# Performance work log

Hardware: AMD Instinct MI355X
Metric: run time of the kernel (lower is better)

The kernel has to match this reference:

```python
import jax, jax.numpy as jnp
import numpy as np

B, L, IN_DIM, H, DK, DV = 4, 512, 256, 8, 32, 32
TEMP = DK ** 0.5  # temperature = d_k ** 0.5
LN_EPS = 1e-6


def setup_inputs() -> dict:
    key = jax.random.key(0)
    ks = jax.random.split(key, 5)
    s = 0.05
    return {
        "x": jax.random.normal(ks[0], (B, L, IN_DIM), jnp.float32),
        "w_q": jax.random.normal(ks[1], (IN_DIM, H * DK), jnp.float32) * s,
        "w_k": jax.random.normal(ks[2], (IN_DIM, H * DK), jnp.float32) * s,
        "w_v": jax.random.normal(ks[3], (IN_DIM, H * DV), jnp.float32) * s,
        "w_fc": jax.random.normal(ks[4], (H * DV, IN_DIM), jnp.float32) * s,
        "ln_gamma": jnp.ones((IN_DIM,), jnp.float32),
        "ln_beta": jnp.zeros((IN_DIM,), jnp.float32),
    }


def reference(x, w_q, w_k, w_v, w_fc, ln_gamma, ln_beta):
    # LayerNorm (biased variance, eps inside sqrt, as in torch.nn.LayerNorm)
    mu = jnp.mean(x, axis=-1, keepdims=True)
    var = jnp.var(x, axis=-1, keepdims=True)
    xn = (x - mu) / jnp.sqrt(var + LN_EPS) * ln_gamma + ln_beta
    residual = xn

    # Projections; torch layout after transpose(1,3) is [B, d, H, L]; per-head slice is [B, d, L].
    # We use [B, H, d, L] which yields identical per-head tensors (vectorized over heads).
    q = (xn @ w_q).reshape(B, L, H, DK).transpose(0, 2, 3, 1) / TEMP  # [B,H,DK,L]
    k = (xn @ w_k).reshape(B, L, H, DK).transpose(0, 2, 3, 1)          # [B,H,DK,L]
    v = (xn @ w_v).reshape(B, L, H, DV).transpose(0, 2, 3, 1)          # [B,H,DV,L]

    # L1 distance scores (note the source's index convention):
    # attn[b,h,i,j] = mean_d |q[b,h,d,j] - k[b,h,d,i]|   -> [B,H,L,L]
    attn = jnp.mean(jnp.abs(q[:, :, :, None, :] - k[:, :, :, :, None]), axis=2)
    attn = jax.nn.softmax(attn, axis=-1)

    # out[b,h,d,i] = sum_j v[b,h,d,j] * attn[b,h,i,j]   (torch: bmm(v, attn^T))
    out = jnp.einsum('bhdj,bhij->bhdi', v, attn)  # [B,H,DV,L]
    out = out.reshape(B, H * DV, L).transpose(0, 2, 1)  # head-major concat -> [B,L,H*DV]
    out = out @ w_fc + residual  # use_gamma=False path; dropout is identity at eval

    # extract_attn_map (no_grad in source)
    am = jax.lax.stop_gradient(attn)
    am = jnp.mean(am, axis=1)          # mean over heads -> [B,L,L]
    am = jnp.sum(am, axis=1)           # sum over key axis -> [B,L]
    mn = jnp.min(am, axis=1, keepdims=True)
    mx = jnp.max(am, axis=1, keepdims=True)
    am = (am - mn) / (mx - mn)
    return out, am
```

## Files before the change

kernel.cpp:

```cpp
#include <hip/hip_runtime.h>
#include <hip/hip_fp16.h>
#include <math.h>

#define BATCH 4
#define SEQ   512
#define IND   256
#define NH    8
#define DKV   32
#define BH    32
#define NTOK  2048

typedef __attribute__((ext_vector_type(8))) short short8v;
typedef __attribute__((ext_vector_type(4))) float floatx4;

__device__ __forceinline__ unsigned f2bf1(float f) {
    unsigned u = __builtin_bit_cast(unsigned, f);
    return (u + 0x7fffu + ((u >> 16) & 1u)) >> 16;
}
__device__ __forceinline__ unsigned f2bf2(float lo, float hi) {
    return f2bf1(lo) | (f2bf1(hi) << 16);
}
__device__ __forceinline__ __half2 habs2_(__half2 x) {
    unsigned u = __builtin_bit_cast(unsigned, x) & 0x7fff7fffu;
    return __builtin_bit_cast(__half2, u);
}
__device__ __forceinline__ __half2 shfl_xor_h2(__half2 x, int m) {
    float f = __builtin_bit_cast(float, x);
    f = __shfl_xor(f, m, 64);
    return __builtin_bit_cast(__half2, f);
}

__global__ __launch_bounds__(256) void lnproj_kernel(
        const float* __restrict__ x,
        const float* __restrict__ gamma, const float* __restrict__ beta,
        const float* __restrict__ wq, const float* __restrict__ wk,
        const float* __restrict__ wv,
        float* __restrict__ xn, float* __restrict__ am,
        __half* __restrict__ Q, __half* __restrict__ K, __half* __restrict__ V) {
    __shared__ __align__(16) unsigned short As[64][264];
    __shared__ __align__(16) unsigned short Bs[2][64][40];
    const int t = threadIdx.x;
    const int m0 = blockIdx.x * 64;
    const int y = blockIdx.y;
    const int which = y >> 2;
    const int n0 = (y & 3) * 64;
    const float* W = (which == 0) ? wq : (which == 1) ? wk : wv;
    __half* O = (which == 0) ? Q : (which == 1) ? K : V;

    {
        const int r = t >> 2, q = t & 3;
        const float* xr = x + (m0 + r) * IND + q * 64;
        float4 xv[16];
        float s = 0.0f, s2 = 0.0f;
        #pragma unroll
        for (int i = 0; i < 16; i++) {
            xv[i] = *(const float4*)&xr[i * 4];
            s  += xv[i].x + xv[i].y + xv[i].z + xv[i].w;
            s2 += xv[i].x * xv[i].x + xv[i].y * xv[i].y
                + xv[i].z * xv[i].z + xv[i].w * xv[i].w;
        }
        s  += __shfl_xor(s, 1, 64);  s  += __shfl_xor(s, 2, 64);
        s2 += __shfl_xor(s2, 1, 64); s2 += __shfl_xor(s2, 2, 64);
        float mu = s * (1.0f / IND);
        float var = s2 * (1.0f / IND) - mu * mu;
        float rinv = rsqrtf(var + 1e-6f);
        const bool dox = (y == 0);
        if (dox && t < 64) am[m0 + t] = 0.0f;
        #pragma unroll
        for (int i = 0; i < 8; i++) {
            float4 a = xv[2 * i], bv = xv[2 * i + 1];
            float4 g0 = *(const float4*)&gamma[q * 64 + i * 8];
            float4 g1 = *(const float4*)&gamma[q * 64 + i * 8 + 4];
            float4 b0 = *(const float4*)&beta[q * 64 + i * 8];
            float4 b1 = *(const float4*)&beta[q * 64 + i * 8 + 4];
            float4 n0v, n1v;
            n0v.x = (a.x - mu) * rinv * g0.x + b0.x;
            n0v.y = (a.y - mu) * rinv * g0.y + b0.y;
            n0v.z = (a.z - mu) * rinv * g0.z + b0.z;
            n0v.w = (a.w - mu) * rinv * g0.w + b0.w;
            n1v.x = (bv.x - mu) * rinv * g1.x + b1.x;
            n1v.y = (bv.y - mu) * rinv * g1.y + b1.y;
            n1v.z = (bv.z - mu) * rinv * g1.z + b1.z;
            n1v.w = (bv.w - mu) * rinv * g1.w + b1.w;
            if (dox) {
                *(float4*)&xn[(m0 + r) * IND + q * 64 + i * 8] = n0v;
                *(float4*)&xn[(m0 + r) * IND + q * 64 + i * 8 + 4] = n1v;
            }
            uint4 pk;
            pk.x = f2bf2(n0v.x, n0v.y); pk.y = f2bf2(n0v.z, n0v.w);
            pk.z = f2bf2(n1v.x, n1v.y); pk.w = f2bf2(n1v.z, n1v.w);
            *(uint4*)&As[r][q * 64 + i * 8] = pk;
        }
    }

    const int w = t >> 6, l = t & 63;
    const int wm = (w >> 1) * 32, wn = (w & 1) * 32;
    const int fr = l & 15, fg = l >> 4;
    floatx4 acc[2][2];
    #pragma unroll
    for (int i = 0; i < 2; i++)
        #pragma unroll
        for (int j = 0; j < 2; j++) acc[i][j] = (floatx4)(0.0f);

    const int kl = t >> 4, nq = t & 15;
    auto stageB = [&](int kt, int buf) {
        float4 b0 = *(const float4*)&W[(kt * 32 + kl) * IND + n0 + nq * 4];
        float4 b1 = *(const float4*)&W[(kt * 32 + 16 + kl) * IND + n0 + nq * 4];
        Bs[buf][nq * 4 + 0][kl] = (unsigned short)f2bf1(b0.x);
        Bs[buf][nq * 4 + 1][kl] = (unsigned short)f2bf1(b0.y);
        Bs[buf][nq * 4 + 2][kl] = (unsigned short)f2bf1(b0.z);
        Bs[buf][nq * 4 + 3][kl] = (unsigned short)f2bf1(b0.w);
        Bs[buf][nq * 4 + 0][kl + 16] = (unsigned short)f2bf1(b1.x);
        Bs[buf][nq * 4 + 1][kl + 16] = (unsigned short)f2bf1(b1.y);
        Bs[buf][nq * 4 + 2][kl + 16] = (unsigned short)f2bf1(b1.z);
        Bs[buf][nq * 4 + 3][kl + 16] = (unsigned short)f2bf1(b1.w);
    };
    stageB(0, 0);
    __syncthreads();
    #pragma unroll
    for (int kt = 0; kt < 8; kt++) {
        if (kt < 7) stageB(kt + 1, (kt + 1) & 1);
        const int buf = kt & 1;
        short8v a0 = *(const short8v*)&As[wm + fr][kt * 32 + fg * 8];
        short8v a1 = *(const short8v*)&As[wm + 16 + fr][kt * 32 + fg * 8];
        short8v b0 = *(const short8v*)&Bs[buf][wn + fr][fg * 8];
        short8v b1 = *(const short8v*)&Bs[buf][wn + 16 + fr][fg * 8];
        acc[0][0] = __builtin_amdgcn_mfma_f32_16x16x32_bf16(a0, b0, acc[0][0], 0, 0, 0);
        acc[0][1] = __builtin_amdgcn_mfma_f32_16x16x32_bf16(a0, b1, acc[0][1], 0, 0, 0);
        acc[1][0] = __builtin_amdgcn_mfma_f32_16x16x32_bf16(a1, b0, acc[1][0], 0, 0, 0);
        acc[1][1] = __builtin_amdgcn_mfma_f32_16x16x32_bf16(a1, b1, acc[1][1], 0, 0, 0);
        __syncthreads();
    }

    const float scale = (which == 0) ? 0.17677669529663687f : 1.0f;
    #pragma unroll
    for (int mi = 0; mi < 2; mi++)
        #pragma unroll
        for (int ni = 0; ni < 2; ni++)
            #pragma unroll
            for (int reg = 0; reg < 4; reg++) {
                int row = m0 + wm + mi * 16 + fg * 4 + reg;
                int col = n0 + wn + ni * 16 + fr;
                int b = row >> 9, ll = row & 511;
                int h = col >> 5, d = col & 31;
                O[(((b << 3) + h) * SEQ + ll) * DKV + d] =
                    __float2half_rn(acc[mi][ni][reg] * scale);
            }
}

__global__ __launch_bounds__(256) void attn_kernel(
        const __half* __restrict__ Qh, const __half* __restrict__ Kh,
        const __half* __restrict__ Vh, float* __restrict__ attn_out,
        float* __restrict__ am) {
    __shared__ __align__(16) __half Th[2][128][40];
    const int t = threadIdx.x;
    const int gy = blockIdx.y;
    const int i0 = blockIdx.x * 16;
    const int b = gy >> 3, h = gy & 7;
    const __half* Qb = Qh + gy * SEQ * DKV;
    const __half* Kb = Kh + gy * SEQ * DKV;
    const __half* Vb = Vh + gy * SEQ * DKV;
    const int g = t >> 5, jl = t & 31;
    const int r0 = t >> 2, ch = t & 3;

    __half2 ka[16], kb[16];
    {
        const float4* pa = (const float4*)(Kb + (i0 + g) * DKV);
        const float4* pb = (const float4*)(Kb + (i0 + g + 8) * DKV);
        #pragma unroll
        for (int c = 0; c < 4; c++) {
            float4 va = pa[c], vb = pb[c];
            const __half2* ha = (const __half2*)&va;
            const __half2* hb = (const __half2*)&vb;
            #pragma unroll
            for (int k = 0; k < 4; k++) { ka[c*4+k] = ha[k]; kb[c*4+k] = hb[k]; }
        }
    }

    float vals_a[16], vals_b[16];
    float4 pre0, pre1;

    pre0 = *(const float4*)(Qb + r0 * DKV + ch * 8);
    pre1 = *(const float4*)(Qb + (r0 + 64) * DKV + ch * 8);
    *(float4*)&Th[0][r0][ch * 8] = pre0;
    *(float4*)&Th[0][r0 + 64][ch * 8] = pre1;
    __syncthreads();
    #pragma unroll
    for (int tile = 0; tile < 4; tile++) {
        const int buf = tile & 1;
        if (tile < 3) {
            pre0 = *(const float4*)(Qb + ((tile+1)*128 + r0) * DKV + ch * 8);
            pre1 = *(const float4*)(Qb + ((tile+1)*128 + r0 + 64) * DKV + ch * 8);
        }
        #pragma unroll
        for (int m = 0; m < 4; m++) {
            const int j = jl + m * 32;
            __half2 z = __float2half2_rn(0.0f);
            __half2 sa0 = z, sa1 = z, sb0 = z, sb1 = z;
            #pragma unroll
            for (int c = 0; c < 4; c++) {
                float4 qv = *(const float4*)&Th[buf][j][c * 8];
                const __half2* q2 = (const __half2*)&qv;
                #pragma unroll
                for (int k = 0; k < 4; k++) {
                    __half2 da = habs2_(__hsub2(q2[k], ka[c*4+k]));
                    __half2 db = habs2_(__hsub2(q2[k], kb[c*4+k]));
                    if (k & 1) { sa1 = __hadd2(sa1, da); sb1 = __hadd2(sb1, db); }
                    else       { sa0 = __hadd2(sa0, da); sb0 = __hadd2(sb0, db); }
                }
            }
            __half2 sa = __hadd2(sa0, sa1), sb = __hadd2(sb0, sb1);
            vals_a[tile*4+m] = (__low2float(sa) + __high2float(sa)) * (1.0f/32.0f);
            vals_b[tile*4+m] = (__low2float(sb) + __high2float(sb)) * (1.0f/32.0f);
        }
        if (tile < 3) {
            *(float4*)&Th[buf ^ 1][r0][ch * 8] = pre0;
            *(float4*)&Th[buf ^ 1][r0 + 64][ch * 8] = pre1;
        }
        __syncthreads();
    }

    float mxa = vals_a[0], mxb = vals_b[0];
    #pragma unroll
    for (int m = 1; m < 16; m++) {
        mxa = fmaxf(mxa, vals_a[m]); mxb = fmaxf(mxb, vals_b[m]);
    }
    #pragma unroll
    for (int s = 1; s <= 16; s <<= 1) {
        mxa = fmaxf(mxa, __shfl_xor(mxa, s, 64));
        mxb = fmaxf(mxb, __shfl_xor(mxb, s, 64));
    }
    float sua = 0.0f, sub = 0.0f;
    #pragma unroll
    for (int m = 0; m < 16; m++) {
        vals_a[m] = __expf(vals_a[m] - mxa); sua += vals_a[m];
        vals_b[m] = __expf(vals_b[m] - mxb); sub += vals_b[m];
    }
    #pragma unroll
    for (int s = 1; s <= 16; s <<= 1) {
        sua += __shfl_xor(sua, s, 64);
        sub += __shfl_xor(sub, s, 64);
    }
    float inva = 1.0f / sua, invb = 1.0f / sub;
    #pragma unroll
    for (int m = 0; m < 16; m++) { vals_a[m] *= inva; vals_b[m] *= invb; }

    __half2 acc_a[16], acc_b[16];
    #pragma unroll
    for (int k = 0; k < 16; k++) {
        acc_a[k] = __float2half2_rn(0.0f);
        acc_b[k] = __float2half2_rn(0.0f);
    }
    pre0 = *(const float4*)(Vb + r0 * DKV + ch * 8);
    pre1 = *(const float4*)(Vb + (r0 + 64) * DKV + ch * 8);
    *(float4*)&Th[0][r0][ch * 8] = pre0;
    *(float4*)&Th[0][r0 + 64][ch * 8] = pre1;
    __syncthreads();
    #pragma unroll
    for (int tile = 0; tile < 4; tile++) {
        const int buf = tile & 1;
        if (tile < 3) {
            pre0 = *(const float4*)(Vb + ((tile+1)*128 + r0) * DKV + ch * 8);
            pre1 = *(const float4*)(Vb + ((tile+1)*128 + r0 + 64) * DKV + ch * 8);
        }
        #pragma unroll
        for (int m = 0; m < 4; m++) {
            const int j = jl + m * 32;
            __half2 pa = __float2half2_rn(vals_a[tile*4+m]);
            __half2 pb = __float2half2_rn(vals_b[tile*4+m]);
            #pragma unroll
            for (int c = 0; c < 4; c++) {
                float4 vv = *(const float4*)&Th[buf][j][c * 8];
                const __half2* v2 = (const __half2*)&vv;
                #pragma unroll
                for (int k = 0; k < 4; k++) {
                    acc_a[c*4+k] = __hfma2(pa, v2[k], acc_a[c*4+k]);
                    acc_b[c*4+k] = __hfma2(pb, v2[k], acc_b[c*4+k]);
                }
            }
        }
        if (tile < 3) {
            *(float4*)&Th[buf ^ 1][r0][ch * 8] = pre0;
            *(float4*)&Th[buf ^ 1][r0 + 64][ch * 8] = pre1;
        }
        __syncthreads();
    }

#define REDSTEP(S, C)                                                      \
    {                                                                      \
        _Pragma("unroll")                                                  \
        for (int k = 0; k < (C); k++) {                                    \
            __half2 sa = (jl & (S)) ? acc_a[k] : acc_a[k + (C)];           \
            __half2 sb = (jl & (S)) ? acc_b[k] : acc_b[k + (C)];           \
            __half2 ra = shfl_xor_h2(sa, (S));                             \
            __half2 rb = shfl_xor_h2(sb, (S));                             \
            __half2 qa = (jl & (S)) ? acc_a[k + (C)] : acc_a[k];           \
            __half2 qb = (jl & (S)) ? acc_b[k + (C)] : acc_b[k];           \
            acc_a[k] = __hadd2(qa, ra);                                    \
            acc_b[k] = __hadd2(qb, rb);                                    \
        }                                                                  \
    }
    REDSTEP(16, 8)
    REDSTEP(8, 4)
    REDSTEP(4, 2)
    REDSTEP(2, 1)
#undef REDSTEP
    acc_a[0] = __hadd2(acc_a[0], shfl_xor_h2(acc_a[0], 1));
    acc_b[0] = __hadd2(acc_b[0], shfl_xor_h2(acc_b[0], 1));
    if (!(jl & 1)) {
        int d2 = (jl >> 1) & 15;
        int col = h * 32 + d2 * 2;
        float2 oa = make_float2(__low2float(acc_a[0]), __high2float(acc_a[0]));
        float2 ob = make_float2(__low2float(acc_b[0]), __high2float(acc_b[0]));
        *(float2*)&attn_out[(b * SEQ + i0 + g) * IND + col] = oa;
        *(float2*)&attn_out[(b * SEQ + i0 + g + 8) * IND + col] = ob;
    }

    float colp[16];
    #pragma unroll
    for (int m = 0; m < 16; m++) {
        float cp = vals_a[m] + vals_b[m];
        cp += __shfl_xor(cp, 32, 64);
        colp[m] = cp;
    }
    float* amw = (float*)&Th[0][0][0];
    const int w = t >> 6;
    if (!(t & 32)) {
        #pragma unroll
        for (int m = 0; m < 16; m++) {
            int j = (m >> 2) * 128 + (m & 3) * 32 + jl;
            amw[w * 512 + j] = colp[m];
        }
    }
    __syncthreads();
    #pragma unroll
    for (int n = 0; n < 2; n++) {
        int j = t + n * 256;
        float s = (amw[j] + amw[512 + j] + amw[1024 + j] + amw[1536 + j]) * 0.125f;
        atomicAdd(&am[b * SEQ + j], s);
    }
}

__global__ __launch_bounds__(256) void fcam_kernel(
        const float* __restrict__ ao, const float* __restrict__ wfc,
        const float* __restrict__ xn, const float* __restrict__ am,
        float* __restrict__ out, float* __restrict__ out_am) {
    __shared__ __align__(16) unsigned short As[64][264];
    __shared__ __align__(16) unsigned short Bs[2][64][40];
    __shared__ float lmn[4], lmx[4];
    const int t = threadIdx.x;

    if (blockIdx.x == 32) {
        int b = blockIdx.y;
        float v0 = am[b * SEQ + t];
        float v1 = am[b * SEQ + t + 256];
        float mn = fminf(v0, v1), mx = fmaxf(v0, v1);
        #pragma unroll
        for (int o = 32; o > 0; o >>= 1) {
            mn = fminf(mn, __shfl_xor(mn, o, 64));
            mx = fmaxf(mx, __shfl_xor(mx, o, 64));
        }
        int w = t >> 6;
        if ((t & 63) == 0) { lmn[w] = mn; lmx[w] = mx; }
        __syncthreads();
        mn = fminf(fminf(lmn[0], lmn[1]), fminf(lmn[2], lmn[3]));
        mx = fmaxf(fmaxf(lmx[0], lmx[1]), fmaxf(lmx[2], lmx[3]));
        float inv = 1.0f / (mx - mn);
        out_am[b * SEQ + t]       = (v0 - mn) * inv;
        out_am[b * SEQ + t + 256] = (v1 - mn) * inv;
        return;
    }

    const int m0 = blockIdx.x * 64;
    const int n0 = blockIdx.y * 64;

    {
        const int r = t >> 2, q = t & 3;
        const float* ar = ao + (m0 + r) * IND + q * 64;
        #pragma unroll
        for (int i = 0; i < 8; i++) {
            float4 a = *(const float4*)&ar[i * 8];
            float4 bv = *(const float4*)&ar[i * 8 + 4];
            uint4 pk;
            pk.x = f2bf2(a.x, a.y);  pk.y = f2bf2(a.z, a.w);
            pk.z = f2bf2(bv.x, bv.y); pk.w = f2bf2(bv.z, bv.w);
            *(uint4*)&As[r][q * 64 + i * 8] = pk;
        }
    }

    const int w = t >> 6, l = t & 63;
    const int wm = (w >> 1) * 32, wn = (w & 1) * 32;
    const int fr = l & 15, fg = l >> 4;
    floatx4 acc[2][2];
    #pragma unroll
    for (int i = 0; i < 2; i++)
        #pragma unroll
        for (int j = 0; j < 2; j++) acc[i][j] = (floatx4)(0.0f);

    const int kl = t >> 4, nq = t & 15;
    auto stageB = [&](int kt, int buf) {
        float4 b0 = *(const float4*)&wfc[(kt * 32 + kl) * IND + n0 + nq * 4];
        float4 b1 = *(const float4*)&wfc[(kt * 32 + 16 + kl) * IND + n0 + nq * 4];
        Bs[buf][nq * 4 + 0][kl] = (unsigned short)f2bf1(b0.x);
        Bs[buf][nq * 4 + 1][kl] = (unsigned short)f2bf1(b0.y);
        Bs[buf][nq * 4 + 2][kl] = (unsigned short)f2bf1(b0.z);
        Bs[buf][nq * 4 + 3][kl] = (unsigned short)f2bf1(b0.w);
        Bs[buf][nq * 4 + 0][kl + 16] = (unsigned short)f2bf1(b1.x);
        Bs[buf][nq * 4 + 1][kl + 16] = (unsigned short)f2bf1(b1.y);
        Bs[buf][nq * 4 + 2][kl + 16] = (unsigned short)f2bf1(b1.z);
        Bs[buf][nq * 4 + 3][kl + 16] = (unsigned short)f2bf1(b1.w);
    };
    stageB(0, 0);
    __syncthreads();
    #pragma unroll
    for (int kt = 0; kt < 8; kt++) {
        if (kt < 7) stageB(kt + 1, (kt + 1) & 1);
        const int buf = kt & 1;
        short8v a0 = *(const short8v*)&As[wm + fr][kt * 32 + fg * 8];
        short8v a1 = *(const short8v*)&As[wm + 16 + fr][kt * 32 + fg * 8];
        short8v b0 = *(const short8v*)&Bs[buf][wn + fr][fg * 8];
        short8v b1 = *(const short8v*)&Bs[buf][wn + 16 + fr][fg * 8];
        acc[0][0] = __builtin_amdgcn_mfma_f32_16x16x32_bf16(a0, b0, acc[0][0], 0, 0, 0);
        acc[0][1] = __builtin_amdgcn_mfma_f32_16x16x32_bf16(a0, b1, acc[0][1], 0, 0, 0);
        acc[1][0] = __builtin_amdgcn_mfma_f32_16x16x32_bf16(a1, b0, acc[1][0], 0, 0, 0);
        acc[1][1] = __builtin_amdgcn_mfma_f32_16x16x32_bf16(a1, b1, acc[1][1], 0, 0, 0);
        __syncthreads();
    }

    #pragma unroll
    for (int mi = 0; mi < 2; mi++)
        #pragma unroll
        for (int ni = 0; ni < 2; ni++)
            #pragma unroll
            for (int reg = 0; reg < 4; reg++) {
                int row = m0 + wm + mi * 16 + fg * 4 + reg;
                int col = n0 + wn + ni * 16 + fr;
                out[row * IND + col] = acc[mi][ni][reg] + xn[row * IND + col];
            }
}

extern "C" void kernel_launch(void* const* d_in, const int* in_sizes, int n_in,
                              void* d_out, int out_size, void* d_ws, size_t ws_size,
                              hipStream_t stream) {
    (void)in_sizes; (void)n_in; (void)out_size; (void)ws_size;
    const float* x     = (const float*)d_in[0];
    const float* w_q   = (const float*)d_in[1];
    const float* w_k   = (const float*)d_in[2];
    const float* w_v   = (const float*)d_in[3];
    const float* w_fc  = (const float*)d_in[4];
    const float* gamma = (const float*)d_in[5];
    const float* beta  = (const float*)d_in[6];
    float* out = (float*)d_out;

    float* ws = (float*)d_ws;
    float* xn = ws;
    float* AO = xn + NTOK * IND;
    float* AM = AO + NTOK * IND;
    __half* Qh = (__half*)(AM + NTOK);
    __half* Kh = Qh + BH * SEQ * DKV;
    __half* Vh = Kh + BH * SEQ * DKV;

    hipLaunchKernelGGL(lnproj_kernel, dim3(32, 12), dim3(256), 0, stream,
                       x, gamma, beta, w_q, w_k, w_v, xn, AM, Qh, Kh, Vh);
    hipLaunchKernelGGL(attn_kernel, dim3(SEQ / 16, BH), dim3(256), 0, stream,
                       Qh, Kh, Vh, AO, AM);
    hipLaunchKernelGGL(fcam_kernel, dim3(33, 4), dim3(256), 0, stream,
                       AO, w_fc, xn, AM, out, out + NTOK * IND);
}
```

Baseline: 67.72 us.

## Move attention PV product to bf16 MFMA with transposed V and single-wave blocks

```diff
diff --git a/kernel.cpp b/kernel.cpp
--- a/kernel.cpp
+++ b/kernel.cpp
@@ -36,7 +36,8 @@
         const float* __restrict__ wq, const float* __restrict__ wk,
         const float* __restrict__ wv,
         float* __restrict__ xn, float* __restrict__ am,
-        __half* __restrict__ Q, __half* __restrict__ K, __half* __restrict__ V) {
+        __half* __restrict__ Q, __half* __restrict__ K,
+        unsigned short* __restrict__ Vt) {
     __shared__ __align__(16) unsigned short As[64][264];
     __shared__ __align__(16) unsigned short Bs[2][64][40];
     const int t = threadIdx.x;
@@ -45,7 +46,6 @@
     const int which = y >> 2;
     const int n0 = (y & 3) * 64;
     const float* W = (which == 0) ? wq : (which == 1) ? wk : wv;
-    __half* O = (which == 0) ? Q : (which == 1) ? K : V;
 
     {
         const int r = t >> 2, q = t & 3;
@@ -143,201 +143,131 @@
                 int col = n0 + wn + ni * 16 + fr;
                 int b = row >> 9, ll = row & 511;
                 int h = col >> 5, d = col & 31;
-                O[(((b << 3) + h) * SEQ + ll) * DKV + d] =
-                    __float2half_rn(acc[mi][ni][reg] * scale);
-            }
-}
-
-__global__ __launch_bounds__(256) void attn_kernel(
+                if (which == 2) {
+                    Vt[(((b << 3) + h) * DKV + d) * SEQ + ll] =
+                        (unsigned short)f2bf1(acc[mi][ni][reg]);
+                } else {
+                    __half* O = (which == 0) ? Q : K;
+                    O[(((b << 3) + h) * SEQ + ll) * DKV + d] =
+                        __float2half_rn(acc[mi][ni][reg] * scale);
+                }
+            }
+}
+
+__global__ __launch_bounds__(64) void attn_kernel(
         const __half* __restrict__ Qh, const __half* __restrict__ Kh,
-        const __half* __restrict__ Vh, float* __restrict__ attn_out,
-        float* __restrict__ am) {
-    __shared__ __align__(16) __half Th[2][128][40];
-    const int t = threadIdx.x;
+        const unsigned short* __restrict__ Vt,
+        float* __restrict__ attn_out, float* __restrict__ am) {
+    const int l = threadIdx.x;
+    const int li = l & 15, jc = l >> 4;
     const int gy = blockIdx.y;
     const int i0 = blockIdx.x * 16;
     const int b = gy >> 3, h = gy & 7;
     const __half* Qb = Qh + gy * SEQ * DKV;
-    const __half* Kb = Kh + gy * SEQ * DKV;
-    const __half* Vb = Vh + gy * SEQ * DKV;
-    const int g = t >> 5, jl = t & 31;
-    const int r0 = t >> 2, ch = t & 3;
-
-    __half2 ka[16], kb[16];
+    const unsigned short* Vb = Vt + gy * DKV * SEQ;
+
+    __half2 kreg[16];
     {
-        const float4* pa = (const float4*)(Kb + (i0 + g) * DKV);
-        const float4* pb = (const float4*)(Kb + (i0 + g + 8) * DKV);
+        const float4* kp = (const float4*)(Kh + (gy * SEQ + i0 + li) * DKV);
         #pragma unroll
         for (int c = 0; c < 4; c++) {
-            float4 va = pa[c], vb = pb[c];
-            const __half2* ha = (const __half2*)&va;
-            const __half2* hb = (const __half2*)&vb;
-            #pragma unroll
-            for (int k = 0; k < 4; k++) { ka[c*4+k] = ha[k]; kb[c*4+k] = hb[k]; }
-        }
-    }
-
-    float vals_a[16], vals_b[16];
-    float4 pre0, pre1;
-
-    pre0 = *(const float4*)(Qb + r0 * DKV + ch * 8);
-    pre1 = *(const float4*)(Qb + (r0 + 64) * DKV + ch * 8);
-    *(float4*)&Th[0][r0][ch * 8] = pre0;
-    *(float4*)&Th[0][r0 + 64][ch * 8] = pre1;
-    __syncthreads();
-    #pragma unroll
-    for (int tile = 0; tile < 4; tile++) {
-        const int buf = tile & 1;
-        if (tile < 3) {
-            pre0 = *(const float4*)(Qb + ((tile+1)*128 + r0) * DKV + ch * 8);
-            pre1 = *(const float4*)(Qb + ((tile+1)*128 + r0 + 64) * DKV + ch * 8);
-        }
-        #pragma unroll
-        for (int m = 0; m < 4; m++) {
-            const int j = jl + m * 32;
+            float4 kv = kp[c];
+            const __half2* k2 = (const __half2*)&kv;
+            #pragma unroll
+            for (int k = 0; k < 4; k++) kreg[c * 4 + k] = k2[k];
+        }
+    }
+
+    __half2 sreg[64];
+    float mx = -1e30f;
+    #pragma unroll
+    for (int jt = 0; jt < 16; jt++) {
+        float sc[8];
+        #pragma unroll
+        for (int c = 0; c < 8; c++) {
+            const int j = jt * 32 + jc * 8 + c;
+            const float4* qp = (const float4*)(Qb + j * DKV);
             __half2 z = __float2half2_rn(0.0f);
-            __half2 sa0 = z, sa1 = z, sb0 = z, sb1 = z;
-            #pragma unroll
-            for (int c = 0; c < 4; c++) {
-                float4 qv = *(const float4*)&Th[buf][j][c * 8];
+            __half2 a0 = z, a1 = z;
+            #pragma unroll
+            for (int cc = 0; cc < 4; cc++) {
+                float4 qv = qp[cc];
                 const __half2* q2 = (const __half2*)&qv;
                 #pragma unroll
                 for (int k = 0; k < 4; k++) {
-                    __half2 da = habs2_(__hsub2(q2[k], ka[c*4+k]));
-                    __half2 db = habs2_(__hsub2(q2[k], kb[c*4+k]));
-                    if (k & 1) { sa1 = __hadd2(sa1, da); sb1 = __hadd2(sb1, db); }
-                    else       { sa0 = __hadd2(sa0, da); sb0 = __hadd2(sb0, db); }
+                    __half2 d2 = habs2_(__hsub2(q2[k], kreg[cc * 4 + k]));
+                    if (k & 1) a1 = __hadd2(a1, d2); else a0 = __hadd2(a0, d2);
                 }
             }
-            __half2 sa = __hadd2(sa0, sa1), sb = __hadd2(sb0, sb1);
-            vals_a[tile*4+m] = (__low2float(sa) + __high2float(sa)) * (1.0f/32.0f);
-            vals_b[tile*4+m] = (__low2float(sb) + __high2float(sb)) * (1.0f/32.0f);
-        }
-        if (tile < 3) {
-            *(float4*)&Th[buf ^ 1][r0][ch * 8] = pre0;
-            *(float4*)&Th[buf ^ 1][r0 + 64][ch * 8] = pre1;
-        }
-        __syncthreads();
-    }
-
-    float mxa = vals_a[0], mxb = vals_b[0];
-    #pragma unroll
-    for (int m = 1; m < 16; m++) {
-        mxa = fmaxf(mxa, vals_a[m]); mxb = fmaxf(mxb, vals_b[m]);
-    }
-    #pragma unroll
-    for (int s = 1; s <= 16; s <<= 1) {
-        mxa = fmaxf(mxa, __shfl_xor(mxa, s, 64));
-        mxb = fmaxf(mxb, __shfl_xor(mxb, s, 64));
-    }
-    float sua = 0.0f, sub = 0.0f;
-    #pragma unroll
-    for (int m = 0; m < 16; m++) {
-        vals_a[m] = __expf(vals_a[m] - mxa); sua += vals_a[m];
-        vals_b[m] = __expf(vals_b[m] - mxb); sub += vals_b[m];
-    }
-    #pragma unroll
-    for (int s = 1; s <= 16; s <<= 1) {
-        sua += __shfl_xor(sua, s, 64);
-        sub += __shfl_xor(sub, s, 64);
-    }
-    float inva = 1.0f / sua, invb = 1.0f / sub;
-    #pragma unroll
-    for (int m = 0; m < 16; m++) { vals_a[m] *= inva; vals_b[m] *= invb; }
-
-    __half2 acc_a[16], acc_b[16];
-    #pragma unroll
-    for (int k = 0; k < 16; k++) {
-        acc_a[k] = __float2half2_rn(0.0f);
-        acc_b[k] = __float2half2_rn(0.0f);
-    }
-    pre0 = *(const float4*)(Vb + r0 * DKV + ch * 8);
-    pre1 = *(const float4*)(Vb + (r0 + 64) * DKV + ch * 8);
-    *(float4*)&Th[0][r0][ch * 8] = pre0;
-    *(float4*)&Th[0][r0 + 64][ch * 8] = pre1;
-    __syncthreads();
-    #pragma unroll
-    for (int tile = 0; tile < 4; tile++) {
-        const int buf = tile & 1;
-        if (tile < 3) {
-            pre0 = *(const float4*)(Vb + ((tile+1)*128 + r0) * DKV + ch * 8);
-            pre1 = *(const float4*)(Vb + ((tile+1)*128 + r0 + 64) * DKV + ch * 8);
-        }
-        #pragma unroll
-        for (int m = 0; m < 4; m++) {
-            const int j = jl + m * 32;
-            __half2 pa = __float2half2_rn(vals_a[tile*4+m]);
-            __half2 pb = __float2half2_rn(vals_b[tile*4+m]);
-            #pragma unroll
-            for (int c = 0; c < 4; c++) {
-                float4 vv = *(const float4*)&Th[buf][j][c * 8];
-                const __half2* v2 = (const __half2*)&vv;
-                #pragma unroll
-                for (int k = 0; k < 4; k++) {
-                    acc_a[c*4+k] = __hfma2(pa, v2[k], acc_a[c*4+k]);
-                    acc_b[c*4+k] = __hfma2(pb, v2[k], acc_b[c*4+k]);
-                }
-            }
-        }
-        if (tile < 3) {
-            *(float4*)&Th[buf ^ 1][r0][ch * 8] = pre0;
-            *(float4*)&Th[buf ^ 1][r0 + 64][ch * 8] = pre1;
-        }
-        __syncthreads();
-    }
-
-#define REDSTEP(S, C)                                                      \
-    {                                                                      \
-        _Pragma("unroll")                                                  \
-        for (int k = 0; k < (C); k++) {                                    \
-            __half2 sa = (jl & (S)) ? acc_a[k] : acc_a[k + (C)];           \
-            __half2 sb = (jl & (S)) ? acc_b[k] : acc_b[k + (C)];           \
-            __half2 ra = shfl_xor_h2(sa, (S));                             \
-            __half2 rb = shfl_xor_h2(sb, (S));                             \
-            __half2 qa = (jl & (S)) ? acc_a[k + (C)] : acc_a[k];           \
-            __half2 qb = (jl & (S)) ? acc_b[k + (C)] : acc_b[k];           \
-            acc_a[k] = __hadd2(qa, ra);                                    \
-            acc_b[k] = __hadd2(qb, rb);                                    \
-        }                                                                  \
-    }
-    REDSTEP(16, 8)
-    REDSTEP(8, 4)
-    REDSTEP(4, 2)
-    REDSTEP(2, 1)
-#undef REDSTEP
-    acc_a[0] = __hadd2(acc_a[0], shfl_xor_h2(acc_a[0], 1));
-    acc_b[0] = __hadd2(acc_b[0], shfl_xor_h2(acc_b[0], 1));
-    if (!(jl & 1)) {
-        int d2 = (jl >> 1) & 15;
-        int col = h * 32 + d2 * 2;
-        float2 oa = make_float2(__low2float(acc_a[0]), __high2float(acc_a[0]));
-        float2 ob = make_float2(__low2float(acc_b[0]), __high2float(acc_b[0]));
-        *(float2*)&attn_out[(b * SEQ + i0 + g) * IND + col] = oa;
-        *(float2*)&attn_out[(b * SEQ + i0 + g + 8) * IND + col] = ob;
-    }
-
-    float colp[16];
-    #pragma unroll
-    for (int m = 0; m < 16; m++) {
-        float cp = vals_a[m] + vals_b[m];
-        cp += __shfl_xor(cp, 32, 64);
-        colp[m] = cp;
-    }
-    float* amw = (float*)&Th[0][0][0];
-    const int w = t >> 6;
-    if (!(t & 32)) {
-        #pragma unroll
-        for (int m = 0; m < 16; m++) {
-            int j = (m >> 2) * 128 + (m & 3) * 32 + jl;
-            amw[w * 512 + j] = colp[m];
-        }
-    }
-    __syncthreads();
-    #pragma unroll
-    for (int n = 0; n < 2; n++) {
-        int j = t + n * 256;
-        float s = (amw[j] + amw[512 + j] + amw[1024 + j] + amw[1536 + j]) * 0.125f;
-        atomicAdd(&am[b * SEQ + j], s);
+            __half2 a = __hadd2(a0, a1);
+            sc[c] = (__low2float(a) + __high2float(a)) * (1.0f / 32.0f);
+            mx = fmaxf(mx, sc[c]);
+        }
+        #pragma unroll
+        for (int q = 0; q < 4; q++)
+            sreg[jt * 4 + q] = __halves2half2(__float2half_rn(sc[2 * q]),
+                                              __float2half_rn(sc[2 * q + 1]));
+    }
+    mx = fmaxf(mx, __shfl_xor(mx, 16, 64));
+    mx = fmaxf(mx, __shfl_xor(mx, 32, 64));
+
+    float su = 0.0f;
+    #pragma unroll
+    for (int r = 0; r < 64; r++) {
+        float lo = __expf(__low2float(sreg[r]) - mx);
+        float hi = __expf(__high2float(sreg[r]) - mx);
+        su += lo + hi;
+        sreg[r] = __halves2half2(__float2half_rn(lo), __float2half_rn(hi));
+    }
+    su += __shfl_xor(su, 16, 64);
+    su += __shfl_xor(su, 32, 64);
+    const float inv = 1.0f / su;
+    #pragma unroll
+    for (int r = 0; r < 64; r++) {
+        float lo = __low2float(sreg[r]) * inv;
+        float hi = __high2float(sreg[r]) * inv;
+        sreg[r] = __halves2half2(__float2half_rn(lo), __float2half_rn(hi));
+    }
+
+    floatx4 oacc[2];
+    oacc[0] = (floatx4)(0.0f); oacc[1] = (floatx4)(0.0f);
+    #pragma unroll
+    for (int jt = 0; jt < 16; jt++) {
+        uint4 pw;
+        pw.x = f2bf2(__low2float(sreg[jt * 4 + 0]), __high2float(sreg[jt * 4 + 0]));
+        pw.y = f2bf2(__low2float(sreg[jt * 4 + 1]), __high2float(sreg[jt * 4 + 1]));
+        pw.z = f2bf2(__low2float(sreg[jt * 4 + 2]), __high2float(sreg[jt * 4 + 2]));
+        pw.w = f2bf2(__low2float(sreg[jt * 4 + 3]), __high2float(sreg[jt * 4 + 3]));
+        short8v pa = __builtin_bit_cast(short8v, pw);
+        #pragma unroll
+        for (int n = 0; n < 2; n++) {
+            short8v bf = *(const short8v*)&Vb[(n * 16 + li) * SEQ + jt * 32 + jc * 8];
+            oacc[n] = __builtin_amdgcn_mfma_f32_16x16x32_bf16(pa, bf, oacc[n], 0, 0, 0);
+        }
+    }
+    #pragma unroll
+    for (int n = 0; n < 2; n++)
+        #pragma unroll
+        for (int r = 0; r < 4; r++)
+            attn_out[(b * SEQ + i0 + jc * 4 + r) * IND + h * 32 + n * 16 + li] =
+                oacc[n][r];
+
+    #pragma unroll
+    for (int S = 1; S <= 8; S <<= 1)
+        #pragma unroll
+        for (int r = 0; r < 64; r++)
+            sreg[r] = __hadd2(sreg[r], shfl_xor_h2(sreg[r], S));
+    if (li == 0) {
+        #pragma unroll
+        for (int jt = 0; jt < 16; jt++)
+            #pragma unroll
+            for (int q = 0; q < 4; q++) {
+                int jp = jt * 32 + jc * 8 + 2 * q;
+                atomicAdd(&am[b * SEQ + jp],
+                          __low2float(sreg[jt * 4 + q]) * 0.125f);
+                atomicAdd(&am[b * SEQ + jp + 1],
+                          __high2float(sreg[jt * 4 + q]) * 0.125f);
+            }
     }
 }
 
@@ -458,12 +388,12 @@
     float* AM = AO + NTOK * IND;
     __half* Qh = (__half*)(AM + NTOK);
     __half* Kh = Qh + BH * SEQ * DKV;
-    __half* Vh = Kh + BH * SEQ * DKV;
+    unsigned short* Vb16 = (unsigned short*)(Kh + BH * SEQ * DKV);
 
     hipLaunchKernelGGL(lnproj_kernel, dim3(32, 12), dim3(256), 0, stream,
-                       x, gamma, beta, w_q, w_k, w_v, xn, AM, Qh, Kh, Vh);
-    hipLaunchKernelGGL(attn_kernel, dim3(SEQ / 16, BH), dim3(256), 0, stream,
-                       Qh, Kh, Vh, AO, AM);
+                       x, gamma, beta, w_q, w_k, w_v, xn, AM, Qh, Kh, Vb16);
+    hipLaunchKernelGGL(attn_kernel, dim3(SEQ / 16, BH), dim3(64), 0, stream,
+                       Qh, Kh, Vb16, AO, AM);
     hipLaunchKernelGGL(fcam_kernel, dim3(33, 4), dim3(256), 0, stream,
                        AO, w_fc, xn, AM, out, out + NTOK * IND);
 }
```

Result: slower. 162.6 us (+140.2%).

## Compute attention PV product with bf16 MFMA using transposed V layout

Applied to the files above, without the earlier changes.

```diff
diff --git a/kernel.cpp b/kernel.cpp
--- a/kernel.cpp
+++ b/kernel.cpp
@@ -24,11 +24,6 @@
     unsigned u = __builtin_bit_cast(unsigned, x) & 0x7fff7fffu;
     return __builtin_bit_cast(__half2, u);
 }
-__device__ __forceinline__ __half2 shfl_xor_h2(__half2 x, int m) {
-    float f = __builtin_bit_cast(float, x);
-    f = __shfl_xor(f, m, 64);
-    return __builtin_bit_cast(__half2, f);
-}
 
 __global__ __launch_bounds__(256) void lnproj_kernel(
         const float* __restrict__ x,
@@ -36,7 +31,8 @@
         const float* __restrict__ wq, const float* __restrict__ wk,
         const float* __restrict__ wv,
         float* __restrict__ xn, float* __restrict__ am,
-        __half* __restrict__ Q, __half* __restrict__ K, __half* __restrict__ V) {
+        __half* __restrict__ Q, __half* __restrict__ K,
+        unsigned short* __restrict__ Vt) {
     __shared__ __align__(16) unsigned short As[64][264];
     __shared__ __align__(16) unsigned short Bs[2][64][40];
     const int t = threadIdx.x;
@@ -45,7 +41,6 @@
     const int which = y >> 2;
     const int n0 = (y & 3) * 64;
     const float* W = (which == 0) ? wq : (which == 1) ? wk : wv;
-    __half* O = (which == 0) ? Q : (which == 1) ? K : V;
 
     {
         const int r = t >> 2, q = t & 3;
@@ -143,24 +138,33 @@
                 int col = n0 + wn + ni * 16 + fr;
                 int b = row >> 9, ll = row & 511;
                 int h = col >> 5, d = col & 31;
-                O[(((b << 3) + h) * SEQ + ll) * DKV + d] =
-                    __float2half_rn(acc[mi][ni][reg] * scale);
+                if (which == 2) {
+                    Vt[(((b << 3) + h) * DKV + d) * SEQ + ll] =
+                        (unsigned short)f2bf1(acc[mi][ni][reg]);
+                } else {
+                    __half* O = (which == 0) ? Q : K;
+                    O[(((b << 3) + h) * SEQ + ll) * DKV + d] =
+                        __float2half_rn(acc[mi][ni][reg] * scale);
+                }
             }
 }
 
 __global__ __launch_bounds__(256) void attn_kernel(
         const __half* __restrict__ Qh, const __half* __restrict__ Kh,
-        const __half* __restrict__ Vh, float* __restrict__ attn_out,
-        float* __restrict__ am) {
+        const unsigned short* __restrict__ Vt,
+        float* __restrict__ attn_out, float* __restrict__ am) {
     __shared__ __align__(16) __half Th[2][128][40];
+    __shared__ __align__(16) unsigned short Pl[16][520];
     const int t = threadIdx.x;
+    const int w = t >> 6, l = t & 63;
+    const int g = t >> 5, jl = t & 31;
+    const int li = l & 15, jc = l >> 4;
     const int gy = blockIdx.y;
     const int i0 = blockIdx.x * 16;
     const int b = gy >> 3, h = gy & 7;
     const __half* Qb = Qh + gy * SEQ * DKV;
     const __half* Kb = Kh + gy * SEQ * DKV;
-    const __half* Vb = Vh + gy * SEQ * DKV;
-    const int g = t >> 5, jl = t & 31;
+    const unsigned short* Vb = Vt + gy * DKV * SEQ;
     const int r0 = t >> 2, ch = t & 3;
 
     __half2 ka[16], kb[16];
@@ -245,99 +249,42 @@
     #pragma unroll
     for (int m = 0; m < 16; m++) { vals_a[m] *= inva; vals_b[m] *= invb; }
 
-    __half2 acc_a[16], acc_b[16];
-    #pragma unroll
-    for (int k = 0; k < 16; k++) {
-        acc_a[k] = __float2half2_rn(0.0f);
-        acc_b[k] = __float2half2_rn(0.0f);
-    }
-    pre0 = *(const float4*)(Vb + r0 * DKV + ch * 8);
-    pre1 = *(const float4*)(Vb + (r0 + 64) * DKV + ch * 8);
-    *(float4*)&Th[0][r0][ch * 8] = pre0;
-    *(float4*)&Th[0][r0 + 64][ch * 8] = pre1;
+    #pragma unroll
+    for (int m = 0; m < 16; m++) {
+        const int j = (m >> 2) * 128 + (m & 3) * 32 + jl;
+        Pl[g][j]     = (unsigned short)f2bf1(vals_a[m]);
+        Pl[g + 8][j] = (unsigned short)f2bf1(vals_b[m]);
+    }
     __syncthreads();
-    #pragma unroll
-    for (int tile = 0; tile < 4; tile++) {
-        const int buf = tile & 1;
-        if (tile < 3) {
-            pre0 = *(const float4*)(Vb + ((tile+1)*128 + r0) * DKV + ch * 8);
-            pre1 = *(const float4*)(Vb + ((tile+1)*128 + r0 + 64) * DKV + ch * 8);
-        }
-        #pragma unroll
-        for (int m = 0; m < 4; m++) {
-            const int j = jl + m * 32;
-            __half2 pa = __float2half2_rn(vals_a[tile*4+m]);
-            __half2 pb = __float2half2_rn(vals_b[tile*4+m]);
+
+    floatx4 oacc[2];
+    oacc[0] = (floatx4)(0.0f); oacc[1] = (floatx4)(0.0f);
+    #pragma unroll
+    for (int jt = 0; jt < 16; jt++) {
+        short8v pa = *(const short8v*)&Pl[li][jt * 32 + jc * 8];
+        #pragma unroll
+        for (int n = 0; n < 2; n++) {
+            short8v bf = *(const short8v*)&Vb[(n * 16 + li) * SEQ + jt * 32 + jc * 8];
+            oacc[n] = __builtin_amdgcn_mfma_f32_16x16x32_bf16(pa, bf, oacc[n], 0, 0, 0);
+        }
+    }
+    if (jc == w) {
+        #pragma unroll
+        for (int n = 0; n < 2; n++)
             #pragma unroll
-            for (int c = 0; c < 4; c++) {
-                float4 vv = *(const float4*)&Th[buf][j][c * 8];
-                const __half2* v2 = (const __half2*)&vv;
-                #pragma unroll
-                for (int k = 0; k < 4; k++) {
-                    acc_a[c*4+k] = __hfma2(pa, v2[k], acc_a[c*4+k]);
-                    acc_b[c*4+k] = __hfma2(pb, v2[k], acc_b[c*4+k]);
-                }
-            }
-        }
-        if (tile < 3) {
-            *(float4*)&Th[buf ^ 1][r0][ch * 8] = pre0;
-            *(float4*)&Th[buf ^ 1][r0 + 64][ch * 8] = pre1;
-        }
-        __syncthreads();
-    }
-
-#define REDSTEP(S, C)                                                      \
-    {                                                                      \
-        _Pragma("unroll")                                                  \
-        for (int k = 0; k < (C); k++) {                                    \
-            __half2 sa = (jl & (S)) ? acc_a[k] : acc_a[k + (C)];           \
-            __half2 sb = (jl & (S)) ? acc_b[k] : acc_b[k + (C)];           \
-            __half2 ra = shfl_xor_h2(sa, (S));                             \
-            __half2 rb = shfl_xor_h2(sb, (S));                             \
-            __half2 qa = (jl & (S)) ? acc_a[k + (C)] : acc_a[k];           \
-            __half2 qb = (jl & (S)) ? acc_b[k + (C)] : acc_b[k];           \
-            acc_a[k] = __hadd2(qa, ra);                                    \
-            acc_b[k] = __hadd2(qb, rb);                                    \
-        }                                                                  \
-    }
-    REDSTEP(16, 8)
-    REDSTEP(8, 4)
-    REDSTEP(4, 2)
-    REDSTEP(2, 1)
-#undef REDSTEP
-    acc_a[0] = __hadd2(acc_a[0], shfl_xor_h2(acc_a[0], 1));
-    acc_b[0] = __hadd2(acc_b[0], shfl_xor_h2(acc_b[0], 1));
-    if (!(jl & 1)) {
-        int d2 = (jl >> 1) & 15;
-        int col = h * 32 + d2 * 2;
-        float2 oa = make_float2(__low2float(acc_a[0]), __high2float(acc_a[0]));
-        float2 ob = make_float2(__low2float(acc_b[0]), __high2float(acc_b[0]));
-        *(float2*)&attn_out[(b * SEQ + i0 + g) * IND + col] = oa;
-        *(float2*)&attn_out[(b * SEQ + i0 + g + 8) * IND + col] = ob;
-    }
-
-    float colp[16];
-    #pragma unroll
-    for (int m = 0; m < 16; m++) {
-        float cp = vals_a[m] + vals_b[m];
-        cp += __shfl_xor(cp, 32, 64);
-        colp[m] = cp;
-    }
-    float* amw = (float*)&Th[0][0][0];
-    const int w = t >> 6;
-    if (!(t & 32)) {
-        #pragma unroll
-        for (int m = 0; m < 16; m++) {
-            int j = (m >> 2) * 128 + (m & 3) * 32 + jl;
-            amw[w * 512 + j] = colp[m];
-        }
-    }
-    __syncthreads();
-    #pragma unroll
-    for (int n = 0; n < 2; n++) {
-        int j = t + n * 256;
-        float s = (amw[j] + amw[512 + j] + amw[1024 + j] + amw[1536 + j]) * 0.125f;
-        atomicAdd(&am[b * SEQ + j], s);
+            for (int r = 0; r < 4; r++)
+                attn_out[(b * SEQ + i0 + jc * 4 + r) * IND + h * 32 + n * 16 + li] =
+                    oacc[n][r];
+    }
+
+    #pragma unroll
+    for (int nn = 0; nn < 2; nn++) {
+        const int j = t + nn * 256;
+        float cs = 0.0f;
+        #pragma unroll
+        for (int i = 0; i < 16; i++)
+            cs += __builtin_bit_cast(float, ((unsigned)Pl[i][j]) << 16);
+        atomicAdd(&am[b * SEQ + j], cs * 0.125f);
     }
 }
 
@@ -458,12 +405,12 @@
     float* AM = AO + NTOK * IND;
     __half* Qh = (__half*)(AM + NTOK);
     __half* Kh = Qh + BH * SEQ * DKV;
-    __half* Vh = Kh + BH * SEQ * DKV;
+    unsigned short* Vb16 = (unsigned short*)(Kh + BH * SEQ * DKV);
 
     hipLaunchKernelGGL(lnproj_kernel, dim3(32, 12), dim3(256), 0, stream,
-                       x, gamma, beta, w_q, w_k, w_v, xn, AM, Qh, Kh, Vh);
-    hipLaunchKernelGGL(attn_kernel, dim3(SEQ / 16, BH), dim3(256), 0, stream,
-                       Qh, Kh, Vh, AO, AM);
+                       x, gamma, beta, w_q, w_k, w_v, xn, AM, Qh, Kh, Vb16);
+    hipLaunchKernelGGL(attn_kernel, dim3(32, 32), dim3(256), 0, stream,
+                       Qh, Kh, Vb16, AO, AM);
     hipLaunchKernelGGL(fcam_kernel, dim3(33, 4), dim3(256), 0, stream,
                        AO, w_fc, xn, AM, out, out + NTOK * IND);
 }
```

Measured after the change: 68.39 us. About the same (+1.0%).

## Load full Q/V head into swizzled LDS once, prefetch V during softmax

Applied to the files above, without the earlier changes.

```diff
diff --git a/kernel.cpp b/kernel.cpp
--- a/kernel.cpp
+++ b/kernel.cpp
@@ -148,11 +148,11 @@
             }
 }
 
-__global__ __launch_bounds__(256) void attn_kernel(
+__global__ __launch_bounds__(256, 4) void attn_kernel(
         const __half* __restrict__ Qh, const __half* __restrict__ Kh,
         const __half* __restrict__ Vh, float* __restrict__ attn_out,
         float* __restrict__ am) {
-    __shared__ __align__(16) __half Th[2][128][40];
+    __shared__ __align__(16) __half Qs[SEQ * DKV];
     const int t = threadIdx.x;
     const int gy = blockIdx.y;
     const int i0 = blockIdx.x * 16;
@@ -161,7 +161,9 @@
     const __half* Kb = Kh + gy * SEQ * DKV;
     const __half* Vb = Vh + gy * SEQ * DKV;
     const int g = t >> 5, jl = t & 31;
-    const int r0 = t >> 2, ch = t & 3;
+
+    auto sw = [](int row, int c) { return row * 4 + (c ^ (row & 3) ^ ((row >> 2) & 3)); };
+    float4* Qd = (float4*)Qs;
 
     __half2 ka[16], kb[16];
     {
@@ -177,47 +179,45 @@
         }
     }
 
+    {
+        const float4* Qg = (const float4*)Qb;
+        #pragma unroll
+        for (int n = 0; n < 8; n++) {
+            int idx = n * 256 + t;
+            int row = idx >> 2, c = idx & 3;
+            Qd[sw(row, c)] = Qg[idx];
+        }
+    }
+    __syncthreads();
+
     float vals_a[16], vals_b[16];
-    float4 pre0, pre1;
-
-    pre0 = *(const float4*)(Qb + r0 * DKV + ch * 8);
-    pre1 = *(const float4*)(Qb + (r0 + 64) * DKV + ch * 8);
-    *(float4*)&Th[0][r0][ch * 8] = pre0;
-    *(float4*)&Th[0][r0 + 64][ch * 8] = pre1;
-    __syncthreads();
-    #pragma unroll
-    for (int tile = 0; tile < 4; tile++) {
-        const int buf = tile & 1;
-        if (tile < 3) {
-            pre0 = *(const float4*)(Qb + ((tile+1)*128 + r0) * DKV + ch * 8);
-            pre1 = *(const float4*)(Qb + ((tile+1)*128 + r0 + 64) * DKV + ch * 8);
-        }
-        #pragma unroll
-        for (int m = 0; m < 4; m++) {
-            const int j = jl + m * 32;
-            __half2 z = __float2half2_rn(0.0f);
-            __half2 sa0 = z, sa1 = z, sb0 = z, sb1 = z;
+    #pragma unroll
+    for (int m = 0; m < 16; m++) {
+        const int j = m * 32 + jl;
+        __half2 z = __float2half2_rn(0.0f);
+        __half2 sa0 = z, sa1 = z, sb0 = z, sb1 = z;
+        #pragma unroll
+        for (int c = 0; c < 4; c++) {
+            float4 qv = Qd[sw(j, c)];
+            const __half2* q2 = (const __half2*)&qv;
             #pragma unroll
-            for (int c = 0; c < 4; c++) {
-                float4 qv = *(const float4*)&Th[buf][j][c * 8];
-                const __half2* q2 = (const __half2*)&qv;
-                #pragma unroll
-                for (int k = 0; k < 4; k++) {
-                    __half2 da = habs2_(__hsub2(q2[k], ka[c*4+k]));
-                    __half2 db = habs2_(__hsub2(q2[k], kb[c*4+k]));
-                    if (k & 1) { sa1 = __hadd2(sa1, da); sb1 = __hadd2(sb1, db); }
-                    else       { sa0 = __hadd2(sa0, da); sb0 = __hadd2(sb0, db); }
-                }
+            for (int k = 0; k < 4; k++) {
+                __half2 da = habs2_(__hsub2(q2[k], ka[c*4+k]));
+                __half2 db = habs2_(__hsub2(q2[k], kb[c*4+k]));
+                if (k & 1) { sa1 = __hadd2(sa1, da); sb1 = __hadd2(sb1, db); }
+                else       { sa0 = __hadd2(sa0, da); sb0 = __hadd2(sb0, db); }
             }
-            __half2 sa = __hadd2(sa0, sa1), sb = __hadd2(sb0, sb1);
-            vals_a[tile*4+m] = (__low2float(sa) + __high2float(sa)) * (1.0f/32.0f);
-            vals_b[tile*4+m] = (__low2float(sb) + __high2float(sb)) * (1.0f/32.0f);
-        }
-        if (tile < 3) {
-            *(float4*)&Th[buf ^ 1][r0][ch * 8] = pre0;
-            *(float4*)&Th[buf ^ 1][r0 + 64][ch * 8] = pre1;
-        }
-        __syncthreads();
+        }
+        __half2 sa = __hadd2(sa0, sa1), sb = __hadd2(sb0, sb1);
+        vals_a[m] = (__low2float(sa) + __high2float(sa)) * (1.0f/32.0f);
+        vals_b[m] = (__low2float(sb) + __high2float(sb)) * (1.0f/32.0f);
+    }
+
+    float4 vreg[8];
+    {
+        const float4* Vg = (const float4*)Vb;
+        #pragma unroll
+        for (int n = 0; n < 8; n++) vreg[n] = Vg[n * 256 + t];
     }
 
     float mxa = vals_a[0], mxb = vals_b[0];
@@ -245,45 +245,36 @@
     #pragma unroll
     for (int m = 0; m < 16; m++) { vals_a[m] *= inva; vals_b[m] *= invb; }
 
+    __syncthreads();
+    #pragma unroll
+    for (int n = 0; n < 8; n++) {
+        int idx = n * 256 + t;
+        int row = idx >> 2, c = idx & 3;
+        Qd[sw(row, c)] = vreg[n];
+    }
+    __syncthreads();
+
     __half2 acc_a[16], acc_b[16];
     #pragma unroll
     for (int k = 0; k < 16; k++) {
         acc_a[k] = __float2half2_rn(0.0f);
         acc_b[k] = __float2half2_rn(0.0f);
     }
-    pre0 = *(const float4*)(Vb + r0 * DKV + ch * 8);
-    pre1 = *(const float4*)(Vb + (r0 + 64) * DKV + ch * 8);
-    *(float4*)&Th[0][r0][ch * 8] = pre0;
-    *(float4*)&Th[0][r0 + 64][ch * 8] = pre1;
-    __syncthreads();
-    #pragma unroll
-    for (int tile = 0; tile < 4; tile++) {
-        const int buf = tile & 1;
-        if (tile < 3) {
-            pre0 = *(const float4*)(Vb + ((tile+1)*128 + r0) * DKV + ch * 8);
-            pre1 = *(const float4*)(Vb + ((tile+1)*128 + r0 + 64) * DKV + ch * 8);
-        }
-        #pragma unroll
-        for (int m = 0; m < 4; m++) {
-            const int j = jl + m * 32;
-            __half2 pa = __float2half2_rn(vals_a[tile*4+m]);
-            __half2 pb = __float2half2_rn(vals_b[tile*4+m]);
+    #pragma unroll
+    for (int m = 0; m < 16; m++) {
+        const int j = m * 32 + jl;
+        __half2 pa = __float2half2_rn(vals_a[m]);
+        __half2 pb = __float2half2_rn(vals_b[m]);
+        #pragma unroll
+        for (int c = 0; c < 4; c++) {
+            float4 vv = Qd[sw(j, c)];
+            const __half2* v2 = (const __half2*)&vv;
             #pragma unroll
-            for (int c = 0; c < 4; c++) {
-                float4 vv = *(const float4*)&Th[buf][j][c * 8];
-                const __half2* v2 = (const __half2*)&vv;
-                #pragma unroll
-                for (int k = 0; k < 4; k++) {
-                    acc_a[c*4+k] = __hfma2(pa, v2[k], acc_a[c*4+k]);
-                    acc_b[c*4+k] = __hfma2(pb, v2[k], acc_b[c*4+k]);
-                }
+            for (int k = 0; k < 4; k++) {
+                acc_a[c*4+k] = __hfma2(pa, v2[k], acc_a[c*4+k]);
+                acc_b[c*4+k] = __hfma2(pb, v2[k], acc_b[c*4+k]);
             }
         }
-        if (tile < 3) {
-            *(float4*)&Th[buf ^ 1][r0][ch * 8] = pre0;
-            *(float4*)&Th[buf ^ 1][r0 + 64][ch * 8] = pre1;
-        }
-        __syncthreads();
     }
 
 #define REDSTEP(S, C)                                                      \
@@ -323,12 +314,13 @@
         cp += __shfl_xor(cp, 32, 64);
         colp[m] = cp;
     }
-    float* amw = (float*)&Th[0][0][0];
+    __syncthreads();
+    float* amw = (float*)Qs;
     const int w = t >> 6;
     if (!(t & 32)) {
         #pragma unroll
         for (int m = 0; m < 16; m++) {
-            int j = (m >> 2) * 128 + (m & 3) * 32 + jl;
+            int j = m * 32 + jl;
             amw[w * 512 + j] = colp[m];
         }
     }
@@ -462,7 +454,7 @@
 
     hipLaunchKernelGGL(lnproj_kernel, dim3(32, 12), dim3(256), 0, stream,
                        x, gamma, beta, w_q, w_k, w_v, xn, AM, Qh, Kh, Vh);
-    hipLaunchKernelGGL(attn_kernel, dim3(SEQ / 16, BH), dim3(256), 0, stream,
+    hipLaunchKernelGGL(attn_kernel, dim3(32, 32), dim3(256), 0, stream,
                        Qh, Kh, Vh, AO, AM);
     hipLaunchKernelGGL(fcam_kernel, dim3(33, 4), dim3(256), 0, stream,
                        AO, w_fc, xn, AM, out, out + NTOK * IND);
```

Measured after the change: 75.32 us. 1.11x slower.
